# Optimization experiments

Measured on AMD Instinct MI355X. Metric: run time of the kernel, lower is better.

## Reference

```python
import jax, jax.numpy as jnp
import numpy as np

K = 0.5   # k constant from init
QS = 0.1  # qs constant from init


def setup_inputs() -> dict:
    key = jax.random.key(0)
    k1, k2, k3 = jax.random.split(key, 3)
    B, OUT, M, IN = 512, 128, 8, 512
    x = jax.random.normal(k1, (B, IN), dtype=jnp.float32)
    W = jax.random.uniform(k2, (OUT, M, IN), dtype=jnp.float32)
    q = jax.random.uniform(k3, (OUT, M, IN), dtype=jnp.float32)
    return {"x": x, "W": W, "q": q}


def reference(x, W, q):
    # x: [B, IN]; W, q: [OUT, M, IN]
    # dendritic: relu(k * (x*W - q)), summed over input dim
    syn = jax.nn.relu(K * (x[:, None, None, :] * W - q))  # [B, OUT, M, IN]
    dend = jax.nn.relu(jnp.sum(syn, axis=3))              # [B, OUT, M]
    soma = jnp.sum(dend, axis=2)                          # [B, OUT]
    return jax.nn.relu(K * (soma - QS))
```

## Files before the change

kernel.cpp:

```cpp
#include <hip/hip_runtime.h>


#define OUTN 128
#define MM   8
#define INN  512

typedef float    f4 __attribute__((ext_vector_type(4)));
typedef _Float16 h2 __attribute__((ext_vector_type(2)));
typedef _Float16 h4 __attribute__((ext_vector_type(4)));
typedef _Float16 h8 __attribute__((ext_vector_type(8)));

__global__ __launch_bounds__(256) void dnm_kernel(
    const float* __restrict__ x,
    const float* __restrict__ W,
    const float* __restrict__ q,
    float* __restrict__ out)
{
    __shared__ _Float16 lds_w[MM * INN];
    __shared__ _Float16 lds_q[MM * INN];

    const int tid  = threadIdx.x;
    const int o    = blockIdx.x >> 5;
    const int bgrp = blockIdx.x & 31;
    const int wave = tid >> 6;
    const int lane = tid & 63;
    const int b0   = bgrp * 16 + wave * 4;
    const int i0   = lane * 8;

    {
        const f4* Wg = (const f4*)(W + (size_t)o * MM * INN);
        const f4* qg = (const f4*)(q + (size_t)o * MM * INN);
        h4* lw = (h4*)lds_w;
        h4* lq = (h4*)lds_q;
        #pragma unroll
        for (int c = 0; c < 4; ++c) {
            const int j = tid + c * 256;
            lw[j] = __builtin_convertvector(Wg[j], h4);
            lq[j] = __builtin_convertvector(qg[j], h4);
        }
    }

    h8 xv[4];
    #pragma unroll
    for (int b = 0; b < 4; ++b) {
        const float* xr = x + (size_t)(b0 + b) * INN + i0;
        f4 lo = *(const f4*)xr;
        f4 hi = *(const f4*)(xr + 4);
        h4 l = __builtin_convertvector(lo, h4);
        h4 h = __builtin_convertvector(hi, h4);
        xv[b] = (h8){l[0], l[1], l[2], l[3], h[0], h[1], h[2], h[3]};
    }

    __syncthreads();

    float acc[4];
    #pragma unroll
    for (int b = 0; b < 4; ++b) acc[b] = 0.0f;

    const h2 one = {(_Float16)1.0f, (_Float16)1.0f};

    #pragma unroll 2
    for (int m = 0; m < MM; ++m) {
        const h8 w8 = *(const h8*)(lds_w + m * INN + i0);
        const h8 q8 = *(const h8*)(lds_q + m * INN + i0);
        #pragma unroll
        for (int b = 0; b < 4; ++b) {
            #pragma unroll
            for (int p = 0; p < 4; ++p) {
                h2 xx = {xv[b][2 * p], xv[b][2 * p + 1]};
                h2 ww = {w8[2 * p], w8[2 * p + 1]};
                h2 qq = {q8[2 * p], q8[2 * p + 1]};
                h2 t = __builtin_elementwise_fma(xx, ww, -qq);
                t = __builtin_elementwise_max(t, (h2)(_Float16)0.0f);
#if __has_builtin(__builtin_amdgcn_fdot2)
                acc[b] = __builtin_amdgcn_fdot2(t, one, acc[b], false);
#else
                acc[b] += (float)t[0] + (float)t[1];
#endif
            }
        }
    }

    #pragma unroll
    for (int b = 0; b < 4; ++b) {
        float v = acc[b];
        v += __shfl_xor(v, 1, 64);
        v += __shfl_xor(v, 2, 64);
        v += __shfl_xor(v, 4, 64);
        v += __shfl_xor(v, 8, 64);
        v += __shfl_xor(v, 16, 64);
        v += __shfl_xor(v, 32, 64);
        if (lane == b) {
            float r = 0.25f * v - 0.05f;
            out[(size_t)(b0 + b) * OUTN + o] = fmaxf(r, 0.0f);
        }
    }
}

extern "C" void kernel_launch(void* const* d_in, const int* in_sizes, int n_in,
                              void* d_out, int out_size, void* d_ws, size_t ws_size,
                              hipStream_t stream) {
    const float* x = (const float*)d_in[0];
    const float* W = (const float*)d_in[1];
    const float* q = (const float*)d_in[2];
    float* out = (float*)d_out;
    dim3 grid(OUTN * 32);
    dim3 block(256);
    dnm_kernel<<<grid, block, 0, stream>>>(x, W, q, out);
}
```

Baseline: 77.70 us.

## Pre-convert inputs to fp16 and tile 2 outputs x 32 batches per block

Adds a pre-pass kernel that converts x, W and q to fp16 in workspace once, so the main kernel no longer repeats the fp32 to fp16 conversion in every block. Each main-kernel block now covers 2 output neurons and 32 batch rows (8 per wave), which increases register-level reuse of x and of the LDS weights and cuts the grid from 4096 to 1024 blocks. W and q tiles are loaded straight into LDS with global_load_lds where the builtin exists, and four relu terms are summed in fp16 before each fdot2. The trade-offs are an extra kernel launch plus a workspace round-trip, and slightly lower accuracy from the partial sums done in fp16.

After: 78.91 us. No clear change (+1.6%).

```diff
diff --git a/kernel.cpp b/kernel.cpp
--- a/kernel.cpp
+++ b/kernel.cpp
@@ -4,107 +4,171 @@
 #define OUTN 128
 #define MM   8
 #define INN  512
+#define BB   512
 
 typedef float    f4 __attribute__((ext_vector_type(4)));
 typedef _Float16 h2 __attribute__((ext_vector_type(2)));
 typedef _Float16 h4 __attribute__((ext_vector_type(4)));
 typedef _Float16 h8 __attribute__((ext_vector_type(8)));
 
-__global__ __launch_bounds__(256) void dnm_kernel(
-    const float* __restrict__ x,
-    const float* __restrict__ W,
-    const float* __restrict__ q,
-    float* __restrict__ out)
+#define XH 0
+#define WH (BB * INN)
+#define QH (WH + OUTN * MM * INN)
+
+__global__ __launch_bounds__(256) void cvt_fp16(
+    const float* __restrict__ x, const float* __restrict__ W,
+    const float* __restrict__ q, _Float16* __restrict__ ws)
 {
-    __shared__ _Float16 lds_w[MM * INN];
-    __shared__ _Float16 lds_q[MM * INN];
+    const int j  = blockIdx.x * 256 + threadIdx.x;
+    const int NX = BB * INN / 8;
+    const int NW = OUTN * MM * INN / 8;
+
+    const float* src;
+    _Float16*    dst;
+    int k;
+    if (j < NX)           { src = x; dst = ws + XH; k = j; }
+    else if (j < NX + NW) { src = W; dst = ws + WH; k = j - NX; }
+    else                  { src = q; dst = ws + QH; k = j - NX - NW; }
+
+    f4 a = ((const f4*)src)[2 * k];
+    f4 b = ((const f4*)src)[2 * k + 1];
+    h4 lo = __builtin_convertvector(a, h4);
+    h4 hi = __builtin_convertvector(b, h4);
+    *(h8*)(dst + (size_t)k * 8) = __builtin_shufflevector(lo, hi, 0, 1, 2, 3, 4, 5, 6, 7);
+}
+
+__device__ __forceinline__ void gload_lds16(const _Float16* g, _Float16* l)
+{
+#if __has_builtin(__builtin_amdgcn_global_load_lds)
+    __builtin_amdgcn_global_load_lds(
+        (const __attribute__((address_space(1))) unsigned int*)g,
+        (__attribute__((address_space(3))) unsigned int*)l, 16, 0, 0);
+#else
+    *(h8*)l = *(const h8*)g;
+#endif
+}
+
+__global__ __launch_bounds__(256) void dnm_main(
+    const _Float16* __restrict__ ws, float* __restrict__ out)
+{
+    __shared__ _Float16 lw[2 * MM * INN];
+    __shared__ _Float16 lq[2 * MM * INN];
 
     const int tid  = threadIdx.x;
-    const int o    = blockIdx.x >> 5;
-    const int bgrp = blockIdx.x & 31;
+    const int og   = blockIdx.x >> 4;
+    const int bgrp = blockIdx.x & 15;
     const int wave = tid >> 6;
     const int lane = tid & 63;
-    const int b0   = bgrp * 16 + wave * 4;
+    const int o0   = og * 2;
+    const int b0   = bgrp * 32 + wave * 8;
     const int i0   = lane * 8;
 
     {
-        const f4* Wg = (const f4*)(W + (size_t)o * MM * INN);
-        const f4* qg = (const f4*)(q + (size_t)o * MM * INN);
-        h4* lw = (h4*)lds_w;
-        h4* lq = (h4*)lds_q;
+        const _Float16* gw = ws + WH + (size_t)o0 * (MM * INN);
+        const _Float16* gq = ws + QH + (size_t)o0 * (MM * INN);
         #pragma unroll
-        for (int c = 0; c < 4; ++c) {
-            const int j = tid + c * 256;
-            lw[j] = __builtin_convertvector(Wg[j], h4);
-            lq[j] = __builtin_convertvector(qg[j], h4);
+        for (int r = 0; r < 4; ++r) {
+            const int h_off = r * 2048 + wave * 512;
+            gload_lds16(gw + h_off + lane * 8, lw + h_off);
+            gload_lds16(gq + h_off + lane * 8, lq + h_off);
         }
     }
 
-    h8 xv[4];
-    #pragma unroll
-    for (int b = 0; b < 4; ++b) {
-        const float* xr = x + (size_t)(b0 + b) * INN + i0;
-        f4 lo = *(const f4*)xr;
-        f4 hi = *(const f4*)(xr + 4);
-        h4 l = __builtin_convertvector(lo, h4);
-        h4 h = __builtin_convertvector(hi, h4);
-        xv[b] = (h8){l[0], l[1], l[2], l[3], h[0], h[1], h[2], h[3]};
+    h8 xv[8];
+    {
+        const _Float16* xb = ws + XH + (size_t)b0 * INN + i0;
+        #pragma unroll
+        for (int b = 0; b < 8; ++b) xv[b] = *(const h8*)(xb + (size_t)b * INN);
     }
 
     __syncthreads();
 
-    float acc[4];
+    float acc[8][2];
     #pragma unroll
-    for (int b = 0; b < 4; ++b) acc[b] = 0.0f;
+    for (int b = 0; b < 8; ++b) {
+        acc[b][0] = 0.0f;
+        acc[b][1] = 0.0f;
+    }
 
-    const h2 one = {(_Float16)1.0f, (_Float16)1.0f};
+    const h2 one  = {(_Float16)1.0f, (_Float16)1.0f};
+    const h2 zero = (h2)(_Float16)0.0f;
 
     #pragma unroll 2
     for (int m = 0; m < MM; ++m) {
-        const h8 w8 = *(const h8*)(lds_w + m * INN + i0);
-        const h8 q8 = *(const h8*)(lds_q + m * INN + i0);
+        h8 w8[2], q8[2];
         #pragma unroll
-        for (int b = 0; b < 4; ++b) {
+        for (int o = 0; o < 2; ++o) {
+            w8[o] = *(const h8*)(lw + o * (MM * INN) + m * INN + i0);
+            q8[o] = *(const h8*)(lq + o * (MM * INN) + m * INN + i0);
+        }
+        #pragma unroll
+        for (int b = 0; b < 8; ++b) {
             #pragma unroll
-            for (int p = 0; p < 4; ++p) {
-                h2 xx = {xv[b][2 * p], xv[b][2 * p + 1]};
-                h2 ww = {w8[2 * p], w8[2 * p + 1]};
-                h2 qq = {q8[2 * p], q8[2 * p + 1]};
-                h2 t = __builtin_elementwise_fma(xx, ww, -qq);
-                t = __builtin_elementwise_max(t, (h2)(_Float16)0.0f);
+            for (int o = 0; o < 2; ++o) {
+                h2 t0, t1, t2, t3;
+                {
+                    h2 xx = __builtin_shufflevector(xv[b], xv[b], 0, 1);
+                    h2 ww = __builtin_shufflevector(w8[o], w8[o], 0, 1);
+                    h2 qq = __builtin_shufflevector(q8[o], q8[o], 0, 1);
+                    t0 = __builtin_elementwise_max(__builtin_elementwise_fma(xx, ww, -qq), zero);
+                }
+                {
+                    h2 xx = __builtin_shufflevector(xv[b], xv[b], 2, 3);
+                    h2 ww = __builtin_shufflevector(w8[o], w8[o], 2, 3);
+                    h2 qq = __builtin_shufflevector(q8[o], q8[o], 2, 3);
+                    t1 = __builtin_elementwise_max(__builtin_elementwise_fma(xx, ww, -qq), zero);
+                }
+                {
+                    h2 xx = __builtin_shufflevector(xv[b], xv[b], 4, 5);
+                    h2 ww = __builtin_shufflevector(w8[o], w8[o], 4, 5);
+                    h2 qq = __builtin_shufflevector(q8[o], q8[o], 4, 5);
+                    t2 = __builtin_elementwise_max(__builtin_elementwise_fma(xx, ww, -qq), zero);
+                }
+                {
+                    h2 xx = __builtin_shufflevector(xv[b], xv[b], 6, 7);
+                    h2 ww = __builtin_shufflevector(w8[o], w8[o], 6, 7);
+                    h2 qq = __builtin_shufflevector(q8[o], q8[o], 6, 7);
+                    t3 = __builtin_elementwise_max(__builtin_elementwise_fma(xx, ww, -qq), zero);
+                }
+                h2 s = (t0 + t1) + (t2 + t3);
 #if __has_builtin(__builtin_amdgcn_fdot2)
-                acc[b] = __builtin_amdgcn_fdot2(t, one, acc[b], false);
+                acc[b][o] = __builtin_amdgcn_fdot2(s, one, acc[b][o], false);
 #else
-                acc[b] += (float)t[0] + (float)t[1];
+                acc[b][o] += (float)s[0] + (float)s[1];
 #endif
             }
         }
     }
 
     #pragma unroll
-    for (int b = 0; b < 4; ++b) {
-        float v = acc[b];
-        v += __shfl_xor(v, 1, 64);
-        v += __shfl_xor(v, 2, 64);
-        v += __shfl_xor(v, 4, 64);
-        v += __shfl_xor(v, 8, 64);
-        v += __shfl_xor(v, 16, 64);
-        v += __shfl_xor(v, 32, 64);
-        if (lane == b) {
-            float r = 0.25f * v - 0.05f;
-            out[(size_t)(b0 + b) * OUTN + o] = fmaxf(r, 0.0f);
+    for (int b = 0; b < 8; ++b) {
+        #pragma unroll
+        for (int o = 0; o < 2; ++o) {
+            float v = acc[b][o];
+            v += __shfl_xor(v, 1, 64);
+            v += __shfl_xor(v, 2, 64);
+            v += __shfl_xor(v, 4, 64);
+            v += __shfl_xor(v, 8, 64);
+            v += __shfl_xor(v, 16, 64);
+            v += __shfl_xor(v, 32, 64);
+            if (lane == (b * 2 + o)) {
+                float r = 0.25f * v - 0.05f;
+                out[(size_t)(b0 + b) * OUTN + (o0 + o)] = fmaxf(r, 0.0f);
+            }
         }
     }
 }
 
 extern "C" void kernel_launch(void* const* d_in, const int* in_sizes, int n_in,
                               void* d_out, int out_size, void* d_ws, size_t ws_size,
-                              hipStream_t stream) {
+                              hipStream_t stream)
+{
     const float* x = (const float*)d_in[0];
     const float* W = (const float*)d_in[1];
     const float* q = (const float*)d_in[2];
     float* out = (float*)d_out;
-    dim3 grid(OUTN * 32);
-    dim3 block(256);
-    dnm_kernel<<<grid, block, 0, stream>>>(x, W, q, out);
+    _Float16* ws = (_Float16*)d_ws;
+
+    cvt_fp16<<<dim3(640), dim3(256), 0, stream>>>(x, W, q, ws);
+    dnm_main<<<dim3(1024), dim3(256), 0, stream>>>(ws, out);
 }
```

## Process eight batch rows per wave, halve grid, sum fp16 pairs before dot

Applied to the files above, without the earlier changes.

Each wave now handles 8 batch rows instead of 4, so every block covers 32 rows and the grid shrinks to 2048 blocks. The W/q tiles staged in LDS, including their fp32-to-fp16 conversion, are reused across twice as many rows, which cuts redundant global loads. The four relu'd half2 terms are summed in fp16 before a single fdot2 per row, replacing four fdot2 calls, and conversions use the packed round-toward-zero instruction. The trade-offs are higher register pressure, fewer blocks in flight, and extra fp16 rounding in the partial sums.

After: 82.15 us. +5.7%, slower.

```diff
diff --git a/kernel.cpp b/kernel.cpp
--- a/kernel.cpp
+++ b/kernel.cpp
@@ -4,11 +4,22 @@
 #define OUTN 128
 #define MM   8
 #define INN  512
+#define BB   512
 
 typedef float    f4 __attribute__((ext_vector_type(4)));
 typedef _Float16 h2 __attribute__((ext_vector_type(2)));
 typedef _Float16 h4 __attribute__((ext_vector_type(4)));
 typedef _Float16 h8 __attribute__((ext_vector_type(8)));
+
+__device__ __forceinline__ h2 pkrtz(float a, float b)
+{
+#if __has_builtin(__builtin_amdgcn_cvt_pkrtz)
+    auto t = __builtin_amdgcn_cvt_pkrtz(a, b);
+    return (h2){(_Float16)t[0], (_Float16)t[1]};
+#else
+    return (h2){(_Float16)a, (_Float16)b};
+#endif
+}
 
 __global__ __launch_bounds__(256) void dnm_kernel(
     const float* __restrict__ x,
@@ -16,73 +27,100 @@
     const float* __restrict__ q,
     float* __restrict__ out)
 {
-    __shared__ _Float16 lds_w[MM * INN];
-    __shared__ _Float16 lds_q[MM * INN];
+    __shared__ _Float16 lw[MM * INN];
+    __shared__ _Float16 lq[MM * INN];
 
     const int tid  = threadIdx.x;
-    const int o    = blockIdx.x >> 5;
-    const int bgrp = blockIdx.x & 31;
+    const int o    = blockIdx.x >> 4;
+    const int bgrp = blockIdx.x & 15;
     const int wave = tid >> 6;
     const int lane = tid & 63;
-    const int b0   = bgrp * 16 + wave * 4;
+    const int b0   = bgrp * 32 + wave * 8;
     const int i0   = lane * 8;
 
     {
         const f4* Wg = (const f4*)(W + (size_t)o * MM * INN);
         const f4* qg = (const f4*)(q + (size_t)o * MM * INN);
-        h4* lw = (h4*)lds_w;
-        h4* lq = (h4*)lds_q;
+        h4* lwv = (h4*)lw;
+        h4* lqv = (h4*)lq;
         #pragma unroll
         for (int c = 0; c < 4; ++c) {
             const int j = tid + c * 256;
-            lw[j] = __builtin_convertvector(Wg[j], h4);
-            lq[j] = __builtin_convertvector(qg[j], h4);
+            f4 a = Wg[j];
+            f4 b = qg[j];
+            h2 a01 = pkrtz(a[0], a[1]);
+            h2 a23 = pkrtz(a[2], a[3]);
+            h2 b01 = pkrtz(b[0], b[1]);
+            h2 b23 = pkrtz(b[2], b[3]);
+            lwv[j] = (h4){a01[0], a01[1], a23[0], a23[1]};
+            lqv[j] = (h4){b01[0], b01[1], b23[0], b23[1]};
         }
     }
 
-    h8 xv[4];
+    h8 xv[8];
     #pragma unroll
-    for (int b = 0; b < 4; ++b) {
+    for (int b = 0; b < 8; ++b) {
         const float* xr = x + (size_t)(b0 + b) * INN + i0;
         f4 lo = *(const f4*)xr;
         f4 hi = *(const f4*)(xr + 4);
-        h4 l = __builtin_convertvector(lo, h4);
-        h4 h = __builtin_convertvector(hi, h4);
-        xv[b] = (h8){l[0], l[1], l[2], l[3], h[0], h[1], h[2], h[3]};
+        h2 p0 = pkrtz(lo[0], lo[1]);
+        h2 p1 = pkrtz(lo[2], lo[3]);
+        h2 p2 = pkrtz(hi[0], hi[1]);
+        h2 p3 = pkrtz(hi[2], hi[3]);
+        xv[b] = (h8){p0[0], p0[1], p1[0], p1[1], p2[0], p2[1], p3[0], p3[1]};
     }
 
     __syncthreads();
 
-    float acc[4];
+    float acc[8];
     #pragma unroll
-    for (int b = 0; b < 4; ++b) acc[b] = 0.0f;
+    for (int b = 0; b < 8; ++b) acc[b] = 0.0f;
 
-    const h2 one = {(_Float16)1.0f, (_Float16)1.0f};
+    const h2 one  = {(_Float16)1.0f, (_Float16)1.0f};
+    const h2 zero = (h2)(_Float16)0.0f;
 
     #pragma unroll 2
     for (int m = 0; m < MM; ++m) {
-        const h8 w8 = *(const h8*)(lds_w + m * INN + i0);
-        const h8 q8 = *(const h8*)(lds_q + m * INN + i0);
+        const h8 w8 = *(const h8*)(lw + m * INN + i0);
+        const h8 q8 = *(const h8*)(lq + m * INN + i0);
         #pragma unroll
-        for (int b = 0; b < 4; ++b) {
-            #pragma unroll
-            for (int p = 0; p < 4; ++p) {
-                h2 xx = {xv[b][2 * p], xv[b][2 * p + 1]};
-                h2 ww = {w8[2 * p], w8[2 * p + 1]};
-                h2 qq = {q8[2 * p], q8[2 * p + 1]};
-                h2 t = __builtin_elementwise_fma(xx, ww, -qq);
-                t = __builtin_elementwise_max(t, (h2)(_Float16)0.0f);
+        for (int b = 0; b < 8; ++b) {
+            h2 t0, t1, t2, t3;
+            {
+                h2 xx = __builtin_shufflevector(xv[b], xv[b], 0, 1);
+                h2 ww = __builtin_shufflevector(w8, w8, 0, 1);
+                h2 qq = __builtin_shufflevector(q8, q8, 0, 1);
+                t0 = __builtin_elementwise_max(__builtin_elementwise_fma(xx, ww, -qq), zero);
+            }
+            {
+                h2 xx = __builtin_shufflevector(xv[b], xv[b], 2, 3);
+                h2 ww = __builtin_shufflevector(w8, w8, 2, 3);
+                h2 qq = __builtin_shufflevector(q8, q8, 2, 3);
+                t1 = __builtin_elementwise_max(__builtin_elementwise_fma(xx, ww, -qq), zero);
+            }
+            {
+                h2 xx = __builtin_shufflevector(xv[b], xv[b], 4, 5);
+                h2 ww = __builtin_shufflevector(w8, w8, 4, 5);
+                h2 qq = __builtin_shufflevector(q8, q8, 4, 5);
+                t2 = __builtin_elementwise_max(__builtin_elementwise_fma(xx, ww, -qq), zero);
+            }
+            {
+                h2 xx = __builtin_shufflevector(xv[b], xv[b], 6, 7);
+                h2 ww = __builtin_shufflevector(w8, w8, 6, 7);
+                h2 qq = __builtin_shufflevector(q8, q8, 6, 7);
+                t3 = __builtin_elementwise_max(__builtin_elementwise_fma(xx, ww, -qq), zero);
+            }
+            h2 s = (t0 + t1) + (t2 + t3);
 #if __has_builtin(__builtin_amdgcn_fdot2)
-                acc[b] = __builtin_amdgcn_fdot2(t, one, acc[b], false);
+            acc[b] = __builtin_amdgcn_fdot2(s, one, acc[b], false);
 #else
-                acc[b] += (float)t[0] + (float)t[1];
+            acc[b] += (float)s[0] + (float)s[1];
 #endif
-            }
         }
     }
 
     #pragma unroll
-    for (int b = 0; b < 4; ++b) {
+    for (int b = 0; b < 8; ++b) {
         float v = acc[b];
         v += __shfl_xor(v, 1, 64);
         v += __shfl_xor(v, 2, 64);
@@ -99,12 +137,13 @@
 
 extern "C" void kernel_launch(void* const* d_in, const int* in_sizes, int n_in,
                               void* d_out, int out_size, void* d_ws, size_t ws_size,
-                              hipStream_t stream) {
+                              hipStream_t stream)
+{
     const float* x = (const float*)d_in[0];
     const float* W = (const float*)d_in[1];
     const float* q = (const float*)d_in[2];
     float* out = (float*)d_out;
-    dim3 grid(OUTN * 32);
+    dim3 grid(OUTN * 16);
     dim3 block(256);
     dnm_kernel<<<grid, block, 0, stream>>>(x, W, q, out);
 }
```
